# Kernel optimization log

Hardware: AMD Instinct MI355X
Metric: run time of the kernel (lower is better)

The kernel has to match this reference:

```python
import jax, jax.numpy as jnp
import numpy as np

T, N, E = 4, 20000, 320000
F_IN, EH, NH, GH, OUT = 12, 32, 64, 64, 1
NUM_LAYERS = 2
EB_IN = (EH + 2 * NH) * 2 + GH  # 384
NB_IN = 2 * NH + 2 * EH + GH    # 256
GB_IN = NH + EH + GH            # 160


def setup_inputs() -> dict:
    key = jax.random.key(0)
    ks = jax.random.split(key, 24)
    f32 = jnp.float32
    def w(k, fan_in, shape):
        return jax.random.normal(k, shape, f32) * (1.0 / np.sqrt(fan_in))
    return {
        "node_attr": jax.random.normal(ks[0], (T, N, F_IN), f32),
        "edge_attr": jax.random.normal(ks[1], (T, E, 1), f32),
        "edge_index": jax.random.randint(ks[2], (2, E), 0, N, jnp.int32),
        "sp_L_vals": jax.random.normal(ks[3], (E,), f32),
        "global_attr": jax.random.normal(ks[4], (1, GH), f32),
        "coeff": jnp.full((1,), 0.1, f32),
        "W_ee": w(ks[5], 1, (1, EH)), "b_ee": jnp.zeros((EH,), f32),
        "W_ne": w(ks[6], F_IN, (F_IN, NH)), "b_ne": jnp.zeros((NH,), f32),
        "W_eb": w(ks[7], EB_IN, (EB_IN, EH)), "b_eb": jnp.zeros((EH,), f32),
        "W_nb": w(ks[8], NB_IN, (NB_IN, NH)), "b_nb": jnp.zeros((NH,), f32),
        "W_gb": w(ks[9], GB_IN, (GB_IN, GH)), "b_gb": jnp.zeros((GH,), f32),
        "W_nd1": w(ks[10], NH, (NH, NH)), "b_nd1": jnp.zeros((NH,), f32),
        "W_nd2": w(ks[11], NH, (NH, OUT)), "b_nd2": jnp.zeros((OUT,), f32),
    }


def _forward(node_attr, edge_attr, edge_index, sp_L_vals, global_attr, coeff,
             W_ee, b_ee, W_ne, b_ne, W_eb, b_eb, W_nb, b_nb, W_gb, b_gb,
             W_nd1, b_nd1, W_nd2, b_nd2):
    relu = jax.nn.relu
    s, r = edge_index[0], edge_index[1]
    seg = lambda v, idx: jax.ops.segment_sum(v, idx, num_segments=N)
    c = coeff[0]

    # encoders
    x_enc = relu(node_attr @ W_ne + b_ne)   # [T,N,NH]
    e_enc = relu(edge_attr @ W_ee + b_ee)   # [T,E,EH]

    def run_gn(xT, eT, g0):
        # recurrent GN core over processing steps; hidden (h_x,h_e,h_g) starts at zeros
        def step(carry, inp):
            h_x, h_e, h_g = carry
            x_in, e_in = inp
            gE = jnp.broadcast_to(h_g, (E, GH))
            # EdgeBlock: [edge_in, edge_h, sender_in, sender_h, recv_in, recv_h, global]
            edge_cat = jnp.concatenate(
                [e_in, h_e, x_in[s], h_x[s], x_in[r], h_x[r], gE], axis=-1)
            e_new = relu(edge_cat @ W_eb + b_eb)              # [E,EH]
            sent = seg(e_new, s)                              # scatter_add by sender
            recv = seg(e_new, r)                              # scatter_add by receiver
            gN = jnp.broadcast_to(h_g, (N, GH))
            node_cat = jnp.concatenate([x_in, h_x, sent, recv, gN], axis=-1)
            x_new = relu(node_cat @ W_nb + b_nb)              # [N,NH]
            # GlobalBlock: scatter_mean == plain mean (single graph)
            g_cat = jnp.concatenate(
                [x_new.mean(0, keepdims=True), e_new.mean(0, keepdims=True), h_g], axis=-1)
            g_new = relu(g_cat @ W_gb + b_gb)                 # [1,GH]
            # physics terms (pde='diff'): time derivative = state update,
            # spatial derivative = coeff * (graph-Laplacian action via sp_L edge weights)
            t_der = x_new - h_x
            s_der = c * seg(sp_L_vals[:, None] * (x_new[s] - x_new[r]), r)
            return (x_new, e_new, g_new), (x_new, e_new, g_new, t_der, s_der)
        carry0 = (jnp.zeros((N, NH), jnp.float32), jnp.zeros((E, EH), jnp.float32), g0)
        _, ys = jax.lax.scan(step, carry0, (xT, eT))
        return ys  # xs[T,N,NH], es[T,E,EH], gs[T,1,GH], td[T,N,NH], sd[T,N,NH]

    xs, es, gs, td, sd = run_gn(x_enc, e_enc, global_attr)
    x_pre = x_enc
    for _ in range(NUM_LAYERS - 1):
        x_res = xs + x_pre          # residual node state feeds next GN layer
        x_pre = x_res
        xs, es, gs, td, sd = run_gn(x_res, es, gs[0])

    x_final = xs + x_pre            # add_residual=True final residual
    h = relu(x_final @ W_nd1 + b_nd1)
    out_nodes = h @ W_nd2 + b_nd2   # [T,N,OUT]
    return out_nodes, td, sd


def reference(node_attr, edge_attr, edge_index, sp_L_vals, global_attr, coeff,
              W_ee, b_ee, W_ne, b_ne, W_eb, b_eb, W_nb, b_nb, W_gb, b_gb,
              W_nd1, b_nd1, W_nd2, b_nd2):
    return _forward(node_attr, edge_attr, edge_index, sp_L_vals, global_attr, coeff,
                    W_ee, b_ee, W_ne, b_ne, W_eb, b_eb, W_nb, b_nb, W_gb, b_gb,
                    W_nd1, b_nd1, W_nd2, b_nd2)
```

## Files before the change

kernel.cpp:

```cpp
#include <hip/hip_runtime.h>


typedef __attribute__((ext_vector_type(8))) short s16x8;
typedef __attribute__((ext_vector_type(4))) float f32x4;

#define T_STEPS 4
#define NN 20000
#define NP 20224
#define NE 320000

__device__ __forceinline__ float bf2f(unsigned short h){
  return __uint_as_float(((unsigned)h)<<16);
}
__device__ __forceinline__ unsigned short f2bf(float f){
  unsigned u = __float_as_uint(f);
  return (unsigned short)((u + 0x7fffu + ((u>>16)&1u)) >> 16);
}
__device__ __forceinline__ float loadIn(const void* p, size_t i, int bf){
  return bf ? bf2f(((const unsigned short*)p)[i]) : ((const float*)p)[i];
}
__device__ __forceinline__ void storeOut(void* o, size_t i, float v, int bf){
  if(bf) ((unsigned short*)o)[i] = f2bf(v);
  else   ((float*)o)[i] = v;
}
__device__ __forceinline__ void load8(const float* __restrict__ p, float* v){
  const float4* q4 = (const float4*)p;
  float4 a = q4[0], b = q4[1];
  v[0]=a.x; v[1]=a.y; v[2]=a.z; v[3]=a.w;
  v[4]=b.x; v[5]=b.y; v[6]=b.z; v[7]=b.w;
}
__device__ __forceinline__ int4 pack8(const float* v){
  unsigned p0 = (unsigned)f2bf(v[0]) | ((unsigned)f2bf(v[1])<<16);
  unsigned p1 = (unsigned)f2bf(v[2]) | ((unsigned)f2bf(v[3])<<16);
  unsigned p2 = (unsigned)f2bf(v[4]) | ((unsigned)f2bf(v[5])<<16);
  unsigned p3 = (unsigned)f2bf(v[6]) | ((unsigned)f2bf(v[7])<<16);
  return make_int4((int)p0,(int)p1,(int)p2,(int)p3);
}
__device__ __forceinline__ void unp8(int4 w, float* a){
  unsigned x;
  x=(unsigned)w.x; a[0]=__uint_as_float(x<<16); a[1]=__uint_as_float(x&0xffff0000u);
  x=(unsigned)w.y; a[2]=__uint_as_float(x<<16); a[3]=__uint_as_float(x&0xffff0000u);
  x=(unsigned)w.z; a[4]=__uint_as_float(x<<16); a[5]=__uint_as_float(x&0xffff0000u);
  x=(unsigned)w.w; a[6]=__uint_as_float(x<<16); a[7]=__uint_as_float(x&0xffff0000u);
}

union I4S8 { int4 i; s16x8 s; };

__global__ void probe_kernel(const void* coeff_in, int* flagp, float* coeff_f){
  unsigned short u = ((const unsigned short*)coeff_in)[0];
  float as_bf = bf2f(u);
  int f = (fabsf(as_bf - 0.1f) < 0.02f) ? 1 : 0;
  *flagp = f;
  *coeff_f = f ? as_bf : ((const float*)coeff_in)[0];
}

struct ConvJob { const void* src; float* dst; int n; };
struct ConvJobs { ConvJob j[16]; int cnt; };

__global__ void conv_kernel(ConvJobs jobs, const int* flagp, float* z, int zn){
  int bf = *flagp;
  int tid = blockIdx.x*blockDim.x + threadIdx.x;
  int stride = gridDim.x*blockDim.x;
  for(int q=0;q<jobs.cnt;q++){
    const void* s = jobs.j[q].src; float* d = jobs.j[q].dst; int n = jobs.j[q].n;
    for(int i=tid;i<n;i+=stride) d[i] = loadIn(s, i, bf);
  }
  for(int i=tid;i<zn;i+=stride) z[i]=0.f;
}

__global__ void csr_hist(const int* __restrict__ ei, int* deg_s, int* deg_r,
                         unsigned short* __restrict__ rank_s,
                         unsigned short* __restrict__ rank_r){
  int e = blockIdx.x*256+threadIdx.x;
  rank_s[e] = (unsigned short)atomicAdd(&deg_s[ei[e]],1);
  rank_r[e] = (unsigned short)atomicAdd(&deg_r[ei[NE+e]],1);
}

__global__ void csr_scan(const int* __restrict__ deg_s, int* __restrict__ off_s,
                         const int* __restrict__ deg_r, int* __restrict__ off_r){
  const int CH = NP/256;
  const int* deg = blockIdx.x ? deg_r : deg_s;
  int* off = blockIdx.x ? off_r : off_s;
  int t = threadIdx.x;
  int base = t*CH;
  int s = 0;
  #pragma unroll 8
  for(int i=0;i<CH;i++) s += deg[base+i];
  int lane = t & 63, w = t >> 6;
  int x = s;
  #pragma unroll
  for(int o=1;o<64;o<<=1){
    int y = __shfl_up(x, o, 64);
    if(lane >= o) x += y;
  }
  __shared__ int wtot[4];
  if(lane==63) wtot[w] = x;
  __syncthreads();
  int wbase = 0;
  #pragma unroll
  for(int k=0;k<3;k++) if(k<w) wbase += wtot[k];
  int acc = wbase + x - s;
  #pragma unroll 8
  for(int i=0;i<CH;i++){
    off[base+i]=acc; acc+=deg[base+i];
  }
  if(t==255) off[NN]=acc;
}

__global__ void csr_fill(const int* __restrict__ ei,
                         const int* __restrict__ s_off, const int* __restrict__ r_off,
                         const unsigned short* __restrict__ rank_s,
                         const unsigned short* __restrict__ rank_r,
                         int* __restrict__ csr_s, int* __restrict__ csr_r,
                         int2* __restrict__ sr2,
                         const void* __restrict__ spL, float* __restrict__ spL_p,
                         const int* flagp){
  int e = blockIdx.x*256+threadIdx.x;
  int s = ei[e], r = ei[NE+e];
  int p = r_off[r] + rank_r[e];
  sr2[p] = make_int2(s,r);
  csr_r[p] = e;
  csr_s[s_off[s]+rank_s[e]] = p;
  spL_p[p] = loadIn(spL, e, *flagp);
}

__global__ void pack_w_kernel(const void* __restrict__ W,
                              unsigned short* __restrict__ P, int KW, int NT,
                              const int* flagp){
  int bf = *flagp;
  int idx = blockIdx.x*blockDim.x + threadIdx.x;
  int total = NT*KW*512;
  if(idx>=total) return;
  int j = idx & 7;
  int lane = (idx>>3) & 63;
  int rest = idx >> 9;
  int kw = rest % KW;
  int nt = rest / KW;
  int k = kw*32 + (lane>>4)*8 + j;
  int n = nt*16 + (lane&15);
  P[idx] = f2bf(loadIn(W, (size_t)k*(NT*16) + n, bf));
}

__global__ void node_enc_kernel(const void* __restrict__ na,
                                const float* __restrict__ W, const float* __restrict__ b,
                                unsigned short* __restrict__ xA, const int* flagp){
  __shared__ float arow[4][12];
  int bf = *flagp;
  int lane = threadIdx.x & 63, nl = threadIdx.x >> 6;
  int row = blockIdx.x*4 + nl;
  if(lane<12) arow[nl][lane] = loadIn(na, (size_t)row*12+lane, bf);
  __syncthreads();
  float acc = b[lane];
  #pragma unroll
  for(int k=0;k<12;k++) acc += arow[nl][k]*W[k*64+lane];
  xA[(size_t)row*64+lane] = f2bf(fmaxf(acc,0.f));
}

__global__ __launch_bounds__(256) void edge_block_mfma(
  const int2* __restrict__ sr2,
  const unsigned short* __restrict__ x_in,
  const unsigned short* __restrict__ h_x,
  const void* __restrict__ e_attr,
  int e_attr_off,
  const int* __restrict__ inv,
  const unsigned short* __restrict__ e_in,
  const unsigned short* __restrict__ h_e,
  const float* __restrict__ g,
  const float* __restrict__ W_ee, const float* __restrict__ b_ee,
  const unsigned short* __restrict__ Wp,
  const float* __restrict__ b_eb,
  unsigned short* __restrict__ e_out,
  float* __restrict__ partial_e,
  const int* flagp)
{
  const int tid = threadIdx.x;
  const int lane = tid&63;
  const int q = lane>>4, m16 = lane&15;
  const int pair = blockIdx.x*4 + (tid>>6);
  const int e0 = pair*32;
  const int eg0 = e0 + m16, eg1 = e0 + 16 + m16;
  const int2 sr0 = sr2[eg0], sr1 = sr2[eg1];
  const int o8 = q*8;
  const int4 z4 = make_int4(0,0,0,0);

  I4S8 A0[12], A1[12];
  if(e_attr){
    int bf = *flagp;
    float a0v = loadIn(e_attr, (size_t)e_attr_off + inv[eg0], bf);
    float a1v = loadIn(e_attr, (size_t)e_attr_off + inv[eg1], bf);
    float v[8];
    #pragma unroll
    for(int j=0;j<8;j++) v[j] = fmaxf(a0v*W_ee[o8+j]+b_ee[o8+j], 0.f);
    A0[0].i = pack8(v);
    #pragma unroll
    for(int j=0;j<8;j++) v[j] = fmaxf(a1v*W_ee[o8+j]+b_ee[o8+j], 0.f);
    A1[0].i = pack8(v);
  } else {
    A0[0].i = ((const int4*)(e_in + (size_t)eg0*32))[q];
    A1[0].i = ((const int4*)(e_in + (size_t)eg1*32))[q];
  }
  A0[1].i = h_e ? ((const int4*)(h_e + (size_t)eg0*32))[q] : z4;
  A1[1].i = h_e ? ((const int4*)(h_e + (size_t)eg1*32))[q] : z4;
  { const int4* p0 = (const int4*)(x_in + (size_t)sr0.x*64);
    const int4* p1 = (const int4*)(x_in + (size_t)sr1.x*64);
    A0[2].i = p0[q]; A1[2].i = p1[q];
    A0[3].i = p0[4+q]; A1[3].i = p1[4+q]; }
  if(h_x){
    const int4* p0 = (const int4*)(h_x + (size_t)sr0.x*64);
    const int4* p1 = (const int4*)(h_x + (size_t)sr1.x*64);
    A0[4].i = p0[q]; A1[4].i = p1[q];
    A0[5].i = p0[4+q]; A1[5].i = p1[4+q];
  } else { A0[4].i=z4; A1[4].i=z4; A0[5].i=z4; A1[5].i=z4; }
  { const int4* p0 = (const int4*)(x_in + (size_t)sr0.y*64);
    const int4* p1 = (const int4*)(x_in + (size_t)sr1.y*64);
    A0[6].i = p0[q]; A1[6].i = p1[q];
    A0[7].i = p0[4+q]; A1[7].i = p1[4+q]; }
  if(h_x){
    const int4* p0 = (const int4*)(h_x + (size_t)sr0.y*64);
    const int4* p1 = (const int4*)(h_x + (size_t)sr1.y*64);
    A0[8].i = p0[q]; A1[8].i = p1[q];
    A0[9].i = p0[4+q]; A1[9].i = p1[4+q];
  } else { A0[8].i=z4; A1[8].i=z4; A0[9].i=z4; A1[9].i=z4; }
  { float v[8];
    load8(g + o8, v);      A0[10].i = pack8(v); A1[10].i = A0[10].i;
    load8(g + 32 + o8, v); A0[11].i = pack8(v); A1[11].i = A0[11].i; }

  f32x4 a00={0.f,0.f,0.f,0.f}, a01={0.f,0.f,0.f,0.f};
  f32x4 a10={0.f,0.f,0.f,0.f}, a11={0.f,0.f,0.f,0.f};
  #pragma unroll
  for(int kw=0;kw<12;kw++){
    s16x8 b0 = *(const s16x8*)(Wp + (size_t)(kw*64 + lane)*8);
    s16x8 b1 = *(const s16x8*)(Wp + (size_t)((12+kw)*64 + lane)*8);
    a00 = __builtin_amdgcn_mfma_f32_16x16x32_bf16(A0[kw].s, b0, a00, 0,0,0);
    a01 = __builtin_amdgcn_mfma_f32_16x16x32_bf16(A0[kw].s, b1, a01, 0,0,0);
    a10 = __builtin_amdgcn_mfma_f32_16x16x32_bf16(A1[kw].s, b0, a10, 0,0,0);
    a11 = __builtin_amdgcn_mfma_f32_16x16x32_bf16(A1[kw].s, b1, a11, 0,0,0);
  }

  float pe0=0.f, pe1=0.f;
  const float bb0 = b_eb[m16], bb1 = b_eb[16+m16];
  #pragma unroll
  for(int r=0;r<4;r++){
    int eg0m = e0 + q*4 + r;
    int eg1m = eg0m + 16;
    float v00 = fmaxf(a00[r]+bb0, 0.f);
    float v01 = fmaxf(a01[r]+bb1, 0.f);
    float v10 = fmaxf(a10[r]+bb0, 0.f);
    float v11 = fmaxf(a11[r]+bb1, 0.f);
    e_out[(size_t)eg0m*32+m16]    = f2bf(v00);
    e_out[(size_t)eg0m*32+16+m16] = f2bf(v01);
    e_out[(size_t)eg1m*32+m16]    = f2bf(v10);
    e_out[(size_t)eg1m*32+16+m16] = f2bf(v11);
    pe0 += v00+v10; pe1 += v01+v11;
  }
  pe0 += __shfl_xor(pe0,16,64); pe0 += __shfl_xor(pe0,32,64);
  pe1 += __shfl_xor(pe1,16,64); pe1 += __shfl_xor(pe1,32,64);
  if(q==0){
    int slot = blockIdx.x & 63;
    atomicAdd(&partial_e[slot*32+m16],    pe0);
    atomicAdd(&partial_e[slot*32+16+m16], pe1);
  }
}

__global__ void aggregate_kernel(const unsigned short* __restrict__ e_new,
  const int* __restrict__ s_off, const int* __restrict__ csr_s,
  const int* __restrict__ r_off,
  unsigned short* __restrict__ sentB, unsigned short* __restrict__ recvB)
{
  int node = blockIdx.x*4 + (threadIdx.x>>6);
  int lane = threadIdx.x & 63;
  int f = lane & 31, j = lane >> 5;
  float aS0=0.f, aS1=0.f, aR0=0.f, aR1=0.f;
  {
    int beg = s_off[node], end = s_off[node+1];
    int i = beg + j;
    for(; i+2<end; i+=4){
      aS0 += bf2f(e_new[(size_t)csr_s[i]*32 + f]);
      aS1 += bf2f(e_new[(size_t)csr_s[i+2]*32 + f]);
    }
    for(; i<end; i+=2)
      aS0 += bf2f(e_new[(size_t)csr_s[i]*32 + f]);
  }
  {
    int beg = r_off[node], end = r_off[node+1];
    int i = beg + j;
    for(; i+2<end; i+=4){
      aR0 += bf2f(e_new[(size_t)i*32 + f]);
      aR1 += bf2f(e_new[(size_t)(i+2)*32 + f]);
    }
    for(; i<end; i+=2)
      aR0 += bf2f(e_new[(size_t)i*32 + f]);
  }
  float accS = aS0+aS1, accR = aR0+aR1;
  accS += __shfl_xor(accS,32,64);
  accR += __shfl_xor(accR,32,64);
  if(j==0){
    sentB[(size_t)node*32+f] = f2bf(accS);
    recvB[(size_t)node*32+f] = f2bf(accR);
  }
}

__global__ __launch_bounds__(256) void node_block_mfma(
  const unsigned short* __restrict__ x_in, const unsigned short* __restrict__ h_x,
  const unsigned short* __restrict__ sentB, const unsigned short* __restrict__ recvB,
  const float* __restrict__ g,
  const unsigned short* __restrict__ Wp,
  const float* __restrict__ b_nb,
  unsigned short* __restrict__ x_out, float* __restrict__ partial_x,
  void* __restrict__ out_base, size_t td_off, int has_td,
  const int* flagp)
{
  const int tid = threadIdx.x, lane = tid&63;
  const int q = lane>>4, m16 = lane&15;
  const int tile = blockIdx.x*4 + (tid>>6);
  if(tile >= NN/16) return;
  const int n0 = tile*16;
  const int ng = n0+m16;
  const int o8 = q*8;
  const int4 z4 = make_int4(0,0,0,0);

  I4S8 A[8];
  { const int4* xp = (const int4*)(x_in + (size_t)ng*64);
    A[0].i = xp[q]; A[1].i = xp[4+q]; }
  if(h_x){ const int4* hp = (const int4*)(h_x + (size_t)ng*64);
    A[2].i = hp[q]; A[3].i = hp[4+q];
  } else { A[2].i = z4; A[3].i = z4; }
  A[4].i = ((const int4*)(sentB + (size_t)ng*32))[q];
  A[5].i = ((const int4*)(recvB + (size_t)ng*32))[q];
  { float v[8];
    load8(g + o8, v);      A[6].i = pack8(v);
    load8(g + 32 + o8, v); A[7].i = pack8(v); }

  f32x4 acc[4];
  #pragma unroll
  for(int nt=0;nt<4;nt++) acc[nt] = (f32x4){0.f,0.f,0.f,0.f};
  #pragma unroll
  for(int kw=0;kw<8;kw++){
    #pragma unroll
    for(int nt=0;nt<4;nt++){
      s16x8 b = *(const s16x8*)(Wp + (size_t)((nt*8+kw)*64 + lane)*8);
      acc[nt] = __builtin_amdgcn_mfma_f32_16x16x32_bf16(A[kw].s, b, acc[nt], 0,0,0);
    }
  }

  int bf = has_td ? *flagp : 0;
  float ps[4] = {0.f,0.f,0.f,0.f};
  #pragma unroll
  for(int r=0;r<4;r++){
    int nodeg = n0 + q*4 + r;
    #pragma unroll
    for(int nt=0;nt<4;nt++){
      int col = nt*16 + m16;
      float vv = fmaxf(acc[nt][r] + b_nb[col], 0.f);
      x_out[(size_t)nodeg*64+col] = f2bf(vv);
      if(has_td){
        float hxv = h_x ? bf2f(h_x[(size_t)nodeg*64+col]) : 0.f;
        storeOut(out_base, td_off + (size_t)nodeg*64+col, vv - hxv, bf);
      }
      ps[nt] += vv;
    }
  }
  #pragma unroll
  for(int nt=0;nt<4;nt++){
    ps[nt] += __shfl_xor(ps[nt],16,64);
    ps[nt] += __shfl_xor(ps[nt],32,64);
  }
  if(q==0){
    int slot = blockIdx.x & 63;
    #pragma unroll
    for(int nt=0;nt<4;nt++)
      atomicAdd(&partial_x[slot*64 + nt*16 + m16], ps[nt]);
  }
}

__global__ void global_block_kernel(float* __restrict__ partial_x,
  float* __restrict__ partial_e, const float* __restrict__ h_g,
  const float* __restrict__ W_gb, const float* __restrict__ b_gb,
  float* __restrict__ g_out)
{
  __shared__ float gcat[160];
  __shared__ float red[4][64];
  int tid = threadIdx.x;
  if(tid<64){
    float sx = 0.f;
    #pragma unroll 8
    for(int i=0;i<64;i++) sx += partial_x[i*64+tid];
    gcat[tid] = sx * (1.0f/(float)NN);
  } else if(tid<96){
    int j = tid-64;
    float se = 0.f;
    #pragma unroll 8
    for(int i=0;i<64;i++) se += partial_e[i*32+j];
    gcat[64+j] = se * (1.0f/(float)NE);
  } else if(tid<160){
    gcat[tid] = h_g[tid-96];
  }
  __syncthreads();
  int j = tid&63, c = tid>>6;
  float acc = 0.f;
  #pragma unroll 8
  for(int k=c*40;k<c*40+40;k++) acc += gcat[k]*W_gb[k*64+j];
  red[c][j] = acc;
  __syncthreads();
  for(int i=tid;i<2048;i+=256) partial_e[i]=0.f;
  for(int i=tid;i<4096;i+=256) partial_x[i]=0.f;
  if(tid<64){
    float a = red[0][tid]+red[1][tid]+red[2][tid]+red[3][tid] + b_gb[tid];
    g_out[tid] = fmaxf(a, 0.f);
  }
}

__global__ void sder_csr_kernel(const int2* __restrict__ sr2,
  const float* __restrict__ spL_p, const unsigned short* __restrict__ x_new,
  const int* __restrict__ r_off,
  const float* __restrict__ coeff, void* __restrict__ out_base, size_t off,
  const int* flagp)
{
  int bf = *flagp;
  int lane = threadIdx.x&63, nl = threadIdx.x>>6;
  int node = blockIdx.x*4+nl;
  float xn = bf2f(x_new[(size_t)node*64+lane]);
  float a0=0.f, a1=0.f, a2=0.f, a3=0.f;
  int beg = r_off[node], end = r_off[node+1];
  int i = beg;
  for(; i+4<=end; i+=4){
    float w1 = spL_p[i],   w2 = spL_p[i+1];
    float w3 = spL_p[i+2], w4 = spL_p[i+3];
    int s1 = sr2[i].x, s2 = sr2[i+1].x, s3 = sr2[i+2].x, s4 = sr2[i+3].x;
    a0 += w1*(bf2f(x_new[(size_t)s1*64+lane])-xn);
    a1 += w2*(bf2f(x_new[(size_t)s2*64+lane])-xn);
    a2 += w3*(bf2f(x_new[(size_t)s3*64+lane])-xn);
    a3 += w4*(bf2f(x_new[(size_t)s4*64+lane])-xn);
  }
  for(; i<end; i++){
    float w1 = spL_p[i];
    a0 += w1*(bf2f(x_new[(size_t)sr2[i].x*64+lane])-xn);
  }
  storeOut(out_base, off + (size_t)node*64+lane, coeff[0]*((a0+a1)+(a2+a3)), bf);
}

__global__ void add_bf16_kernel(const unsigned short* __restrict__ a,
  const unsigned short* __restrict__ b, unsigned short* __restrict__ c, int n){
  int i = blockIdx.x*blockDim.x+threadIdx.x;
  int stride = gridDim.x*blockDim.x;
  for(;i<n;i+=stride) c[i] = f2bf(bf2f(a[i])+bf2f(b[i]));
}

__global__ __launch_bounds__(256) void decoder_kernel(
  const unsigned short* __restrict__ xs, const unsigned short* __restrict__ xr,
  const unsigned short* __restrict__ WpD,
  const float* __restrict__ b1, const float* __restrict__ W2,
  const float* __restrict__ b2,
  void* __restrict__ out_base, const int* flagp)
{
  const int tid=threadIdx.x, lane=tid&63;
  const int q=lane>>4, m16=lane&15;
  const int tile = blockIdx.x*4 + (tid>>6);
  const int row0 = tile*16;
  const int rg = row0 + m16;

  I4S8 A[2];
  #pragma unroll
  for(int kw=0;kw<2;kw++){
    int4 xa = ((const int4*)(xs + (size_t)rg*64 + kw*32))[q];
    int4 xb = ((const int4*)(xr + (size_t)rg*64 + kw*32))[q];
    float va[8], vb[8], v[8];
    unp8(xa, va); unp8(xb, vb);
    #pragma unroll
    for(int j=0;j<8;j++) v[j] = va[j]+vb[j];
    A[kw].i = pack8(v);
  }

  f32x4 acc[4];
  #pragma unroll
  for(int nt=0;nt<4;nt++) acc[nt] = (f32x4){0.f,0.f,0.f,0.f};
  #pragma unroll
  for(int kw=0;kw<2;kw++){
    #pragma unroll
    for(int nt=0;nt<4;nt++){
      s16x8 b = *(const s16x8*)(WpD + (size_t)((nt*2+kw)*64 + lane)*8);
      acc[nt] = __builtin_amdgcn_mfma_f32_16x16x32_bf16(A[kw].s, b, acc[nt], 0,0,0);
    }
  }

  float val[4];
  #pragma unroll
  for(int r=0;r<4;r++){
    float s = 0.f;
    #pragma unroll
    for(int nt=0;nt<4;nt++){
      int col = nt*16 + m16;
      s += fmaxf(acc[nt][r] + b1[col], 0.f) * W2[col];
    }
    val[r] = s;
  }
  #pragma unroll
  for(int o=1;o<16;o<<=1){
    #pragma unroll
    for(int r=0;r<4;r++) val[r] += __shfl_xor(val[r], o, 64);
  }
  if(m16==0){
    int bf = *flagp;
    float bb = b2[0];
    #pragma unroll
    for(int r=0;r<4;r++)
      storeOut(out_base, (size_t)(row0 + q*4 + r), val[r] + bb, bf);
  }
}

extern "C" void kernel_launch(void* const* d_in, const int* in_sizes, int n_in,
                              void* d_out, int out_size, void* d_ws, size_t ws_size,
                              hipStream_t stream){
  const void* node_attr = d_in[0];
  const void* edge_attr = d_in[1];
  const int*  ei        = (const int*)d_in[2];
  const void* spL       = d_in[3];
  const void* gattr     = d_in[4];
  const void* coeff_in  = d_in[5];
  const void* W_ee_in = d_in[6];  const void* b_ee_in = d_in[7];
  const void* W_ne_in = d_in[8];  const void* b_ne_in = d_in[9];
  const void* W_eb_in = d_in[10]; const void* b_eb_in = d_in[11];
  const void* W_nb_in = d_in[12]; const void* b_nb_in = d_in[13];
  const void* W_gb_in = d_in[14]; const void* b_gb_in = d_in[15];
  const void* W_nd1_in= d_in[16]; const void* b_nd1_in= d_in[17];
  const void* W_nd2_in= d_in[18]; const void* b_nd2_in= d_in[19];

  float* ws = (float*)d_ws;
  float* W_ee_f = ws;             float* b_ee_f = W_ee_f+32;
  float* W_ne_f = b_ee_f+32;      float* b_ne_f = W_ne_f+768;
  float* W_gb_f = b_ne_f+64;      float* b_gb_f = W_gb_f+10240;
  float* W_nd1_f= b_gb_f+64;      float* b_nd1_f= W_nd1_f+4096;
  float* W_nd2_f= b_nd1_f+64;     float* b_nd2_f= W_nd2_f+64;
  float* b_eb_f = b_nd2_f+1;      float* b_nb_f = b_eb_f+32;
  float* coeff_f= b_nb_f+64;
  int*   flagp  = (int*)(ws + 15523);
  float* gbuf   = ws + 15524;
  float* part_e = ws + 16100;
  float* part_x = part_e + 2048;
  int*   deg_s  = (int*)(part_x + 4096);
  int*   deg_r  = deg_s + NP;
  int*   s_off  = deg_r + NP;
  int*   r_off  = s_off + NP+1;
  unsigned short* rank_s = (unsigned short*)(r_off + NP+1);
  unsigned short* rank_r = rank_s + NE;
  int*   csr_s  = (int*)(rank_r + NE);
  int*   csr_r  = csr_s + NE;
  float* spL_p  = (float*)(csr_r + NE);
  size_t iend   = (size_t)((int*)(spL_p + NE) - (int*)ws);
  iend = (iend + 3) & ~(size_t)3;
  int2*  sr2    = (int2*)(ws + iend);
  unsigned short* sentB = (unsigned short*)(sr2 + NE);
  unsigned short* recvB = sentB + (size_t)NN*32;
  unsigned short* eBuf  = recvB + (size_t)NN*32;
  unsigned short* xA    = eBuf + (size_t)T_STEPS*NE*32;
  unsigned short* xB    = xA + (size_t)T_STEPS*NN*64;
  unsigned short* xC    = xB + (size_t)T_STEPS*NN*64;
  unsigned short* WpE   = xC + (size_t)T_STEPS*NN*64;
  unsigned short* WpN   = WpE + 12288;
  unsigned short* WpD   = WpN + 16384;

  probe_kernel<<<1,1,0,stream>>>(coeff_in, flagp, coeff_f);

  ConvJobs jobs; int c=0;
  auto add=[&](const void* s, float* d, int n){ jobs.j[c].src=s; jobs.j[c].dst=d; jobs.j[c].n=n; c++; };
  add(W_ee_in,W_ee_f,32);   add(b_ee_in,b_ee_f,32);
  add(W_ne_in,W_ne_f,768);  add(b_ne_in,b_ne_f,64);
  add(W_gb_in,W_gb_f,10240);add(b_gb_in,b_gb_f,64);
  add(W_nd1_in,W_nd1_f,4096);add(b_nd1_in,b_nd1_f,64);
  add(W_nd2_in,W_nd2_f,64); add(b_nd2_in,b_nd2_f,1);
  add(b_eb_in,b_eb_f,32);   add(b_nb_in,b_nb_f,64);
  add(gattr,gbuf,64);
  jobs.cnt=c;
  conv_kernel<<<64,256,0,stream>>>(jobs, flagp, part_e, 2048+4096+2*NP);

  csr_hist<<<NE/256,256,0,stream>>>(ei, deg_s, deg_r, rank_s, rank_r);
  csr_scan<<<2,256,0,stream>>>(deg_s, s_off, deg_r, r_off);
  csr_fill<<<NE/256,256,0,stream>>>(ei, s_off, r_off, rank_s, rank_r,
      csr_s, csr_r, sr2, spL, spL_p, flagp);

  pack_w_kernel<<<48,256,0,stream>>>(W_eb_in, WpE, 12, 2, flagp);
  pack_w_kernel<<<64,256,0,stream>>>(W_nb_in, WpN, 8, 4, flagp);
  pack_w_kernel<<<16,256,0,stream>>>(W_nd1_in, WpD, 2, 4, flagp);

  node_enc_kernel<<<T_STEPS*NN/4,256,0,stream>>>(node_attr, W_ne_f, b_ne_f, xA, flagp);

  const size_t td_base = (size_t)T_STEPS*NN;
  const size_t sd_base = td_base + (size_t)T_STEPS*NN*64;

  for(int layer=0; layer<2; layer++){
    for(int t=0;t<T_STEPS;t++){
      const unsigned short* x_in = (layer==0? xA : xC) + (size_t)t*NN*64;
      const unsigned short* h_x  = (t>0)? xB + (size_t)(t-1)*NN*64 : nullptr;
      const unsigned short* h_e  = (t>0)? eBuf + (size_t)(t-1)*NE*32 : nullptr;
      const float* gptr = (layer==0)? gbuf + t*64
                                    : (t==0? gbuf+1*64 : gbuf+(4+t)*64);
      float*       gout = (layer==0)? gbuf+(1+t)*64 : gbuf+(5+t)*64;
      const void*  eat  = (layer==0)? edge_attr : nullptr;
      const unsigned short* e_in = (layer==0)? nullptr : eBuf + (size_t)t*NE*32;
      unsigned short*       e_out= eBuf + (size_t)t*NE*32;

      edge_block_mfma<<<NE/128,256,0,stream>>>(sr2, x_in, h_x, eat, t*NE, csr_r,
          e_in, h_e, gptr, W_ee_f, b_ee_f, WpE, b_eb_f, e_out, part_e, flagp);

      aggregate_kernel<<<NN/4,256,0,stream>>>(e_out, s_off, csr_s, r_off,
          sentB, recvB);

      unsigned short* x_out = xB + (size_t)t*NN*64;
      size_t td_off = td_base + (size_t)t*NN*64;
      node_block_mfma<<<(NN/16+3)/4,256,0,stream>>>(x_in, h_x, sentB, recvB, gptr,
          WpN, b_nb_f, x_out, part_x, d_out, td_off, (layer==1)?1:0, flagp);

      global_block_kernel<<<1,256,0,stream>>>(part_x, part_e, gptr, W_gb_f, b_gb_f, gout);

      if(layer==1){
        sder_csr_kernel<<<NN/4,256,0,stream>>>(sr2, spL_p, x_out, r_off,
            coeff_f, d_out, sd_base + (size_t)t*NN*64, flagp);
      }
    }
    if(layer==0){
      add_bf16_kernel<<<2048,256,0,stream>>>(xA, xB, xC, T_STEPS*NN*64);
    }
  }

  decoder_kernel<<<(T_STEPS*NN/16+3)/4,256,0,stream>>>(xB, xC, WpD,
      b_nd1_f, W_nd2_f, b_nd2_f, d_out, flagp);
}
```

Baseline: 845.7 us.

## Scatter edge outputs into sender-sorted copy and fuse global block into node kernel

The edge kernel now also writes each new edge feature into a second buffer ordered by sender, so the aggregate kernel reads contiguous rows for both the sender and receiver sums instead of gathering through csr_s indices. The aggregate kernel loads 4 bf16 values per lane in vector loads and reduces across 8 edge lanes with shuffles. The global-block kernel is folded into the node kernel through a last-block-done counter, which removes one launch per step. In exchange there is an extra 20 MB scattered write per step, plus a threadfence and an atomic counter on every block.

Measured after the change: 1.102 ms. 30.4% more time.

```diff
diff --git a/kernel.cpp b/kernel.cpp
--- a/kernel.cpp
+++ b/kernel.cpp
@@ -111,7 +111,7 @@
                          const int* __restrict__ s_off, const int* __restrict__ r_off,
                          const unsigned short* __restrict__ rank_s,
                          const unsigned short* __restrict__ rank_r,
-                         int* __restrict__ csr_s, int* __restrict__ csr_r,
+                         int* __restrict__ pos_s, int* __restrict__ csr_r,
                          int2* __restrict__ sr2,
                          const void* __restrict__ spL, float* __restrict__ spL_p,
                          const int* flagp){
@@ -120,7 +120,7 @@
   int p = r_off[r] + rank_r[e];
   sr2[p] = make_int2(s,r);
   csr_r[p] = e;
-  csr_s[s_off[s]+rank_s[e]] = p;
+  pos_s[p] = s_off[s]+rank_s[e];
   spL_p[p] = loadIn(spL, e, *flagp);
 }
 
@@ -163,6 +163,7 @@
   const void* __restrict__ e_attr,
   int e_attr_off,
   const int* __restrict__ inv,
+  const int* __restrict__ pos_s,
   const unsigned short* __restrict__ e_in,
   const unsigned short* __restrict__ h_e,
   const float* __restrict__ g,
@@ -170,6 +171,7 @@
   const unsigned short* __restrict__ Wp,
   const float* __restrict__ b_eb,
   unsigned short* __restrict__ e_out,
+  unsigned short* __restrict__ e_sent,
   float* __restrict__ partial_e,
   const int* flagp)
 {
@@ -243,14 +245,21 @@
   for(int r=0;r<4;r++){
     int eg0m = e0 + q*4 + r;
     int eg1m = eg0m + 16;
+    int sp0 = pos_s[eg0m];
+    int sp1 = pos_s[eg1m];
     float v00 = fmaxf(a00[r]+bb0, 0.f);
     float v01 = fmaxf(a01[r]+bb1, 0.f);
     float v10 = fmaxf(a10[r]+bb0, 0.f);
     float v11 = fmaxf(a11[r]+bb1, 0.f);
-    e_out[(size_t)eg0m*32+m16]    = f2bf(v00);
-    e_out[(size_t)eg0m*32+16+m16] = f2bf(v01);
-    e_out[(size_t)eg1m*32+m16]    = f2bf(v10);
-    e_out[(size_t)eg1m*32+16+m16] = f2bf(v11);
+    unsigned short b00=f2bf(v00), b01=f2bf(v01), b10=f2bf(v10), b11=f2bf(v11);
+    e_out[(size_t)eg0m*32+m16]    = b00;
+    e_out[(size_t)eg0m*32+16+m16] = b01;
+    e_out[(size_t)eg1m*32+m16]    = b10;
+    e_out[(size_t)eg1m*32+16+m16] = b11;
+    e_sent[(size_t)sp0*32+m16]    = b00;
+    e_sent[(size_t)sp0*32+16+m16] = b01;
+    e_sent[(size_t)sp1*32+m16]    = b10;
+    e_sent[(size_t)sp1*32+16+m16] = b11;
     pe0 += v00+v10; pe1 += v01+v11;
   }
   pe0 += __shfl_xor(pe0,16,64); pe0 += __shfl_xor(pe0,32,64);
@@ -262,41 +271,51 @@
   }
 }
 
-__global__ void aggregate_kernel(const unsigned short* __restrict__ e_new,
-  const int* __restrict__ s_off, const int* __restrict__ csr_s,
-  const int* __restrict__ r_off,
+__global__ void aggregate_kernel(const unsigned short* __restrict__ e_recv,
+  const unsigned short* __restrict__ e_sent,
+  const int* __restrict__ s_off, const int* __restrict__ r_off,
   unsigned short* __restrict__ sentB, unsigned short* __restrict__ recvB)
 {
   int node = blockIdx.x*4 + (threadIdx.x>>6);
   int lane = threadIdx.x & 63;
-  int f = lane & 31, j = lane >> 5;
-  float aS0=0.f, aS1=0.f, aR0=0.f, aR1=0.f;
+  int c4 = (lane & 7) * 4;
+  int jr = lane >> 3;
+  float s0=0.f,s1=0.f,s2=0.f,s3=0.f;
+  float r0=0.f,r1=0.f,r2=0.f,r3=0.f;
   {
     int beg = s_off[node], end = s_off[node+1];
-    int i = beg + j;
-    for(; i+2<end; i+=4){
-      aS0 += bf2f(e_new[(size_t)csr_s[i]*32 + f]);
-      aS1 += bf2f(e_new[(size_t)csr_s[i+2]*32 + f]);
-    }
-    for(; i<end; i+=2)
-      aS0 += bf2f(e_new[(size_t)csr_s[i]*32 + f]);
+    for(int i=beg+jr; i<end; i+=8){
+      uint2 w = *(const uint2*)(e_sent + (size_t)i*32 + c4);
+      s0 += __uint_as_float(w.x<<16);
+      s1 += __uint_as_float(w.x&0xffff0000u);
+      s2 += __uint_as_float(w.y<<16);
+      s3 += __uint_as_float(w.y&0xffff0000u);
+    }
   }
   {
     int beg = r_off[node], end = r_off[node+1];
-    int i = beg + j;
-    for(; i+2<end; i+=4){
-      aR0 += bf2f(e_new[(size_t)i*32 + f]);
-      aR1 += bf2f(e_new[(size_t)(i+2)*32 + f]);
-    }
-    for(; i<end; i+=2)
-      aR0 += bf2f(e_new[(size_t)i*32 + f]);
-  }
-  float accS = aS0+aS1, accR = aR0+aR1;
-  accS += __shfl_xor(accS,32,64);
-  accR += __shfl_xor(accR,32,64);
-  if(j==0){
-    sentB[(size_t)node*32+f] = f2bf(accS);
-    recvB[(size_t)node*32+f] = f2bf(accR);
+    for(int i=beg+jr; i<end; i+=8){
+      uint2 w = *(const uint2*)(e_recv + (size_t)i*32 + c4);
+      r0 += __uint_as_float(w.x<<16);
+      r1 += __uint_as_float(w.x&0xffff0000u);
+      r2 += __uint_as_float(w.y<<16);
+      r3 += __uint_as_float(w.y&0xffff0000u);
+    }
+  }
+  #pragma unroll
+  for(int o=8;o<64;o<<=1){
+    s0 += __shfl_xor(s0,o,64); s1 += __shfl_xor(s1,o,64);
+    s2 += __shfl_xor(s2,o,64); s3 += __shfl_xor(s3,o,64);
+    r0 += __shfl_xor(r0,o,64); r1 += __shfl_xor(r1,o,64);
+    r2 += __shfl_xor(r2,o,64); r3 += __shfl_xor(r3,o,64);
+  }
+  if(jr==0){
+    unsigned slo = (unsigned)f2bf(s0) | ((unsigned)f2bf(s1)<<16);
+    unsigned shi = (unsigned)f2bf(s2) | ((unsigned)f2bf(s3)<<16);
+    unsigned rlo = (unsigned)f2bf(r0) | ((unsigned)f2bf(r1)<<16);
+    unsigned rhi = (unsigned)f2bf(r2) | ((unsigned)f2bf(r3)<<16);
+    *(uint2*)(sentB + (size_t)node*32 + c4) = make_uint2(slo,shi);
+    *(uint2*)(recvB + (size_t)node*32 + c4) = make_uint2(rlo,rhi);
   }
 }
 
@@ -308,102 +327,109 @@
   const float* __restrict__ b_nb,
   unsigned short* __restrict__ x_out, float* __restrict__ partial_x,
   void* __restrict__ out_base, size_t td_off, int has_td,
+  float* __restrict__ partial_e,
+  const float* __restrict__ W_gb, const float* __restrict__ b_gb,
+  float* __restrict__ g_out, int* __restrict__ cnt,
   const int* flagp)
 {
   const int tid = threadIdx.x, lane = tid&63;
   const int q = lane>>4, m16 = lane&15;
   const int tile = blockIdx.x*4 + (tid>>6);
-  if(tile >= NN/16) return;
-  const int n0 = tile*16;
-  const int ng = n0+m16;
-  const int o8 = q*8;
-  const int4 z4 = make_int4(0,0,0,0);
-
-  I4S8 A[8];
-  { const int4* xp = (const int4*)(x_in + (size_t)ng*64);
-    A[0].i = xp[q]; A[1].i = xp[4+q]; }
-  if(h_x){ const int4* hp = (const int4*)(h_x + (size_t)ng*64);
-    A[2].i = hp[q]; A[3].i = hp[4+q];
-  } else { A[2].i = z4; A[3].i = z4; }
-  A[4].i = ((const int4*)(sentB + (size_t)ng*32))[q];
-  A[5].i = ((const int4*)(recvB + (size_t)ng*32))[q];
-  { float v[8];
-    load8(g + o8, v);      A[6].i = pack8(v);
-    load8(g + 32 + o8, v); A[7].i = pack8(v); }
-
-  f32x4 acc[4];
-  #pragma unroll
-  for(int nt=0;nt<4;nt++) acc[nt] = (f32x4){0.f,0.f,0.f,0.f};
-  #pragma unroll
-  for(int kw=0;kw<8;kw++){
+  const bool active = (tile < NN/16);
+  if(active){
+    const int n0 = tile*16;
+    const int ng = n0+m16;
+    const int o8 = q*8;
+    const int4 z4 = make_int4(0,0,0,0);
+
+    I4S8 A[8];
+    { const int4* xp = (const int4*)(x_in + (size_t)ng*64);
+      A[0].i = xp[q]; A[1].i = xp[4+q]; }
+    if(h_x){ const int4* hp = (const int4*)(h_x + (size_t)ng*64);
+      A[2].i = hp[q]; A[3].i = hp[4+q];
+    } else { A[2].i = z4; A[3].i = z4; }
+    A[4].i = ((const int4*)(sentB + (size_t)ng*32))[q];
+    A[5].i = ((const int4*)(recvB + (size_t)ng*32))[q];
+    { float v[8];
+      load8(g + o8, v);      A[6].i = pack8(v);
+      load8(g + 32 + o8, v); A[7].i = pack8(v); }
+
+    f32x4 acc[4];
+    #pragma unroll
+    for(int nt=0;nt<4;nt++) acc[nt] = (f32x4){0.f,0.f,0.f,0.f};
+    #pragma unroll
+    for(int kw=0;kw<8;kw++){
+      #pragma unroll
+      for(int nt=0;nt<4;nt++){
+        s16x8 b = *(const s16x8*)(Wp + (size_t)((nt*8+kw)*64 + lane)*8);
+        acc[nt] = __builtin_amdgcn_mfma_f32_16x16x32_bf16(A[kw].s, b, acc[nt], 0,0,0);
+      }
+    }
+
+    int bf = has_td ? *flagp : 0;
+    float ps[4] = {0.f,0.f,0.f,0.f};
+    #pragma unroll
+    for(int r=0;r<4;r++){
+      int nodeg = n0 + q*4 + r;
+      #pragma unroll
+      for(int nt=0;nt<4;nt++){
+        int col = nt*16 + m16;
+        float vv = fmaxf(acc[nt][r] + b_nb[col], 0.f);
+        x_out[(size_t)nodeg*64+col] = f2bf(vv);
+        if(has_td){
+          float hxv = h_x ? bf2f(h_x[(size_t)nodeg*64+col]) : 0.f;
+          storeOut(out_base, td_off + (size_t)nodeg*64+col, vv - hxv, bf);
+        }
+        ps[nt] += vv;
+      }
+    }
     #pragma unroll
     for(int nt=0;nt<4;nt++){
-      s16x8 b = *(const s16x8*)(Wp + (size_t)((nt*8+kw)*64 + lane)*8);
-      acc[nt] = __builtin_amdgcn_mfma_f32_16x16x32_bf16(A[kw].s, b, acc[nt], 0,0,0);
-    }
-  }
-
-  int bf = has_td ? *flagp : 0;
-  float ps[4] = {0.f,0.f,0.f,0.f};
-  #pragma unroll
-  for(int r=0;r<4;r++){
-    int nodeg = n0 + q*4 + r;
-    #pragma unroll
-    for(int nt=0;nt<4;nt++){
-      int col = nt*16 + m16;
-      float vv = fmaxf(acc[nt][r] + b_nb[col], 0.f);
-      x_out[(size_t)nodeg*64+col] = f2bf(vv);
-      if(has_td){
-        float hxv = h_x ? bf2f(h_x[(size_t)nodeg*64+col]) : 0.f;
-        storeOut(out_base, td_off + (size_t)nodeg*64+col, vv - hxv, bf);
-      }
-      ps[nt] += vv;
-    }
-  }
-  #pragma unroll
-  for(int nt=0;nt<4;nt++){
-    ps[nt] += __shfl_xor(ps[nt],16,64);
-    ps[nt] += __shfl_xor(ps[nt],32,64);
-  }
-  if(q==0){
-    int slot = blockIdx.x & 63;
-    #pragma unroll
-    for(int nt=0;nt<4;nt++)
-      atomicAdd(&partial_x[slot*64 + nt*16 + m16], ps[nt]);
-  }
-}
-
-__global__ void global_block_kernel(float* __restrict__ partial_x,
-  float* __restrict__ partial_e, const float* __restrict__ h_g,
-  const float* __restrict__ W_gb, const float* __restrict__ b_gb,
-  float* __restrict__ g_out)
-{
+      ps[nt] += __shfl_xor(ps[nt],16,64);
+      ps[nt] += __shfl_xor(ps[nt],32,64);
+    }
+    if(q==0){
+      int slot = blockIdx.x & 63;
+      #pragma unroll
+      for(int nt=0;nt<4;nt++)
+        atomicAdd(&partial_x[slot*64 + nt*16 + m16], ps[nt]);
+    }
+  }
+
+  __threadfence();
+  __shared__ int lastFlag;
+  if(tid==0) lastFlag = (atomicAdd(cnt,1) == (int)gridDim.x - 1);
+  __syncthreads();
+  if(!lastFlag) return;
+
   __shared__ float gcat[160];
   __shared__ float red[4][64];
-  int tid = threadIdx.x;
   if(tid<64){
     float sx = 0.f;
     #pragma unroll 8
-    for(int i=0;i<64;i++) sx += partial_x[i*64+tid];
+    for(int i=0;i<64;i++)
+      sx += __hip_atomic_load(&partial_x[i*64+tid], __ATOMIC_RELAXED, __HIP_MEMORY_SCOPE_AGENT);
     gcat[tid] = sx * (1.0f/(float)NN);
   } else if(tid<96){
     int j = tid-64;
     float se = 0.f;
     #pragma unroll 8
-    for(int i=0;i<64;i++) se += partial_e[i*32+j];
+    for(int i=0;i<64;i++)
+      se += __hip_atomic_load(&partial_e[i*32+j], __ATOMIC_RELAXED, __HIP_MEMORY_SCOPE_AGENT);
     gcat[64+j] = se * (1.0f/(float)NE);
   } else if(tid<160){
-    gcat[tid] = h_g[tid-96];
+    gcat[tid] = g[tid-96];
   }
   __syncthreads();
-  int j = tid&63, c = tid>>6;
-  float acc = 0.f;
+  int j = tid&63, cc = tid>>6;
+  float acc2 = 0.f;
   #pragma unroll 8
-  for(int k=c*40;k<c*40+40;k++) acc += gcat[k]*W_gb[k*64+j];
-  red[c][j] = acc;
+  for(int k=cc*40;k<cc*40+40;k++) acc2 += gcat[k]*W_gb[k*64+j];
+  red[cc][j] = acc2;
   __syncthreads();
   for(int i=tid;i<2048;i+=256) partial_e[i]=0.f;
   for(int i=tid;i<4096;i+=256) partial_x[i]=0.f;
+  if(tid==0) __hip_atomic_store(cnt, 0, __ATOMIC_RELAXED, __HIP_MEMORY_SCOPE_AGENT);
   if(tid<64){
     float a = red[0][tid]+red[1][tid]+red[2][tid]+red[3][tid] + b_gb[tid];
     g_out[tid] = fmaxf(a, 0.f);
@@ -535,7 +561,9 @@
   float* coeff_f= b_nb_f+64;
   int*   flagp  = (int*)(ws + 15523);
   float* gbuf   = ws + 15524;
-  float* part_e = ws + 16100;
+  float* zbase  = ws + 16100;
+  int*   cnt    = (int*)zbase;
+  float* part_e = zbase + 4;
   float* part_x = part_e + 2048;
   int*   deg_s  = (int*)(part_x + 4096);
   int*   deg_r  = deg_s + NP;
@@ -543,8 +571,8 @@
   int*   r_off  = s_off + NP+1;
   unsigned short* rank_s = (unsigned short*)(r_off + NP+1);
   unsigned short* rank_r = rank_s + NE;
-  int*   csr_s  = (int*)(rank_r + NE);
-  int*   csr_r  = csr_s + NE;
+  int*   pos_s  = (int*)(rank_r + NE);
+  int*   csr_r  = pos_s + NE;
   float* spL_p  = (float*)(csr_r + NE);
   size_t iend   = (size_t)((int*)(spL_p + NE) - (int*)ws);
   iend = (iend + 3) & ~(size_t)3;
@@ -558,6 +586,7 @@
   unsigned short* WpE   = xC + (size_t)T_STEPS*NN*64;
   unsigned short* WpN   = WpE + 12288;
   unsigned short* WpD   = WpN + 16384;
+  unsigned short* eSent = WpD + 4096;
 
   probe_kernel<<<1,1,0,stream>>>(coeff_in, flagp, coeff_f);
 
@@ -571,12 +600,12 @@
   add(b_eb_in,b_eb_f,32);   add(b_nb_in,b_nb_f,64);
   add(gattr,gbuf,64);
   jobs.cnt=c;
-  conv_kernel<<<64,256,0,stream>>>(jobs, flagp, part_e, 2048+4096+2*NP);
+  conv_kernel<<<64,256,0,stream>>>(jobs, flagp, zbase, 4+2048+4096+2*NP);
 
   csr_hist<<<NE/256,256,0,stream>>>(ei, deg_s, deg_r, rank_s, rank_r);
   csr_scan<<<2,256,0,stream>>>(deg_s, s_off, deg_r, r_off);
   csr_fill<<<NE/256,256,0,stream>>>(ei, s_off, r_off, rank_s, rank_r,
-      csr_s, csr_r, sr2, spL, spL_p, flagp);
+      pos_s, csr_r, sr2, spL, spL_p, flagp);
 
   pack_w_kernel<<<48,256,0,stream>>>(W_eb_in, WpE, 12, 2, flagp);
   pack_w_kernel<<<64,256,0,stream>>>(W_nb_in, WpN, 8, 4, flagp);
@@ -600,17 +629,17 @@
       unsigned short*       e_out= eBuf + (size_t)t*NE*32;
 
       edge_block_mfma<<<NE/128,256,0,stream>>>(sr2, x_in, h_x, eat, t*NE, csr_r,
-          e_in, h_e, gptr, W_ee_f, b_ee_f, WpE, b_eb_f, e_out, part_e, flagp);
-
-      aggregate_kernel<<<NN/4,256,0,stream>>>(e_out, s_off, csr_s, r_off,
+          pos_s, e_in, h_e, gptr, W_ee_f, b_ee_f, WpE, b_eb_f, e_out, eSent,
+          part_e, flagp);
+
+      aggregate_kernel<<<NN/4,256,0,stream>>>(e_out, eSent, s_off, r_off,
           sentB, recvB);
 
       unsigned short* x_out = xB + (size_t)t*NN*64;
       size_t td_off = td_base + (size_t)t*NN*64;
       node_block_mfma<<<(NN/16+3)/4,256,0,stream>>>(x_in, h_x, sentB, recvB, gptr,
-          WpN, b_nb_f, x_out, part_x, d_out, td_off, (layer==1)?1:0, flagp);
-
-      global_block_kernel<<<1,256,0,stream>>>(part_x, part_e, gptr, W_gb_f, b_gb_f, gout);
+          WpN, b_nb_f, x_out, part_x, d_out, td_off, (layer==1)?1:0,
+          part_e, W_gb_f, b_gb_f, gout, cnt, flagp);
 
       if(layer==1){
         sder_csr_kernel<<<NN/4,256,0,stream>>>(sr2, spL_p, x_out, r_off,
```
